# Optimization experiments

Measured on AMD Instinct MI355X. Metric: run time of the kernel, lower is better.

Reference implementation:

```python
import math
import jax, jax.numpy as jnp
import numpy as np

DIM = 1024
NUM_HEADS = 16
HEAD_DIM = DIM // NUM_HEADS
SCALE = HEAD_DIM ** -0.5
ROPE_BASE = 10000.0


def _rope(x):
    # x: [b, h, t, d]; rotate-half RoPE as in the torch module
    b, h, t, d = x.shape
    half = d // 2
    freqs = jnp.exp(-math.log(ROPE_BASE) * jnp.arange(half, dtype=jnp.float32) / half)
    pos = jnp.arange(t, dtype=jnp.float32)
    angles = pos[:, None] * freqs[None, :]          # [t, half]
    sin = jnp.sin(angles)[None, None, :, :]
    cos = jnp.cos(angles)[None, None, :, :]
    x1, x2 = x[..., :half], x[..., half:]
    return jnp.concatenate([x1 * cos - x2 * sin, x1 * sin + x2 * cos], axis=-1)


def setup_inputs() -> dict:
    key = jax.random.key(0)
    k1, k2, k3, k4 = jax.random.split(key, 4)
    b, t = 2, 2048
    x = jax.random.normal(k1, (b, t, DIM), dtype=jnp.float32)
    # nn.Linear(dim, 3*dim, bias=False): store as [in, out] for x @ W
    w_qkv = jax.random.normal(k2, (DIM, 3 * DIM), dtype=jnp.float32) * (DIM ** -0.5)
    w_proj = jax.random.normal(k3, (DIM, DIM), dtype=jnp.float32) * (DIM ** -0.5)
    b_proj = jax.random.normal(k4, (DIM,), dtype=jnp.float32) * 0.02
    return {"x": x, "w_qkv": w_qkv, "w_proj": w_proj, "b_proj": b_proj}


def reference(x, w_qkv, w_proj, b_proj):
    b, t, c = x.shape
    h, hd = NUM_HEADS, HEAD_DIM
    qkv = (x @ w_qkv).reshape(b, t, 3, h, hd)
    qkv = jnp.transpose(qkv, (2, 0, 3, 1, 4))      # [3, b, h, t, hd]
    q, k, v = qkv[0], qkv[1], qkv[2]
    q, k = _rope(q), _rope(k)
    attn = jnp.einsum('bhqd,bhkd->bhqk', q, k) * SCALE
    causal_mask = jnp.triu(jnp.ones((t, t), dtype=bool), k=1)
    attn = jnp.where(causal_mask[None, None], -jnp.inf, attn)
    attn = jax.nn.softmax(attn, axis=-1)
    out = jnp.einsum('bhqk,bhkd->bhqd', attn, v)
    out = jnp.transpose(out, (0, 2, 1, 3)).reshape(b, t, c)
    return out @ w_proj + b_proj
```

## Files before the change

kernel.cpp:

```cpp
#include <hip/hip_runtime.h>
#include <math.h>

typedef unsigned short u16;
typedef unsigned int u32;
typedef __bf16 bfrag8 __attribute__((ext_vector_type(8)));
typedef float f32x4 __attribute__((ext_vector_type(4)));

#define B_ 2
#define T_ 2048
#define H_ 16
#define D_ 64
#define C_ 1024
#define NQKV_ 3072

#define MFMA_BF16(a, b, c) __builtin_amdgcn_mfma_f32_16x16x32_bf16((a), (b), (c), 0, 0, 0)

__device__ __forceinline__ u16 f2bf(float f) {
  u32 u = __builtin_bit_cast(u32, f);
  u += 0x7fffu + ((u >> 16) & 1u);
  return (u16)(u >> 16);
}

__device__ __forceinline__ float exp2_fast(float x) {
#if __has_builtin(__builtin_amdgcn_exp2f)
  return __builtin_amdgcn_exp2f(x);
#else
  return __expf(x * 0.6931471805599453f);
#endif
}

__device__ __forceinline__ void load_lds16(const u16* gp, u16* lp) {
  __builtin_amdgcn_global_load_lds(
      (const __attribute__((address_space(1))) u32*)(const void*)gp,
      (__attribute__((address_space(3))) u32*)(void*)lp, 16, 0, 0);
}

__global__ __launch_bounds__(256) void prep(const float* __restrict__ x,
                                            u16* __restrict__ xb,
                                            const float* __restrict__ wqkv,
                                            u16* __restrict__ wqkvT,
                                            const float* __restrict__ wproj,
                                            u16* __restrict__ wprojT) {
  int bid = blockIdx.x;
  int tid = threadIdx.x;
  __shared__ u16 tile[64][65];
  if (bid < 2048) {
    size_t i = ((size_t)bid * 256 + tid) * 8;
    const float* s = x + i;
    float4 a = *(const float4*)s, b = *(const float4*)(s + 4);
    union { uint4 v; u16 h[8]; } t;
    t.h[0] = f2bf(a.x); t.h[1] = f2bf(a.y); t.h[2] = f2bf(a.z); t.h[3] = f2bf(a.w);
    t.h[4] = f2bf(b.x); t.h[5] = f2bf(b.y); t.h[6] = f2bf(b.z); t.h[7] = f2bf(b.w);
    *(uint4*)(xb + i) = t.v;
    return;
  }
  const float* src;
  u16* dst;
  int N, bx, by;
  if (bid < 2816) {
    int rel = bid - 2048;
    src = wqkv; dst = wqkvT; N = NQKV_;
    bx = (rel % 48) * 64; by = (rel / 48) * 64;
  } else {
    int rel = bid - 2816;
    src = wproj; dst = wprojT; N = C_;
    bx = (rel & 15) * 64; by = (rel >> 4) * 64;
  }
  for (int idx = tid; idx < 4096; idx += 256) {
    int r = idx >> 6, c = idx & 63;
    tile[r][c] = f2bf(src[(size_t)(by + r) * N + bx + c]);
  }
  __syncthreads();
  for (int idx = tid; idx < 4096; idx += 256) {
    int r = idx >> 6, c = idx & 63;
    dst[(size_t)(bx + r) * C_ + by + c] = tile[c][r];
  }
}

__global__ __launch_bounds__(256) void gemm_qkv_rope(const u16* __restrict__ X,
                                                     const u16* __restrict__ WT,
                                                     u16* __restrict__ qb,
                                                     u16* __restrict__ kb,
                                                     u16* __restrict__ vtb) {
  const int K = C_;
  __shared__ __align__(16) u16 As[2][128 * 64];
  __shared__ __align__(16) u16 Bs[2][128 * 64];
  int tid = threadIdx.x;
  int lane = tid & 63, wave = tid >> 6;
  int quad = lane >> 4, lr = lane & 15;
  int m0 = blockIdx.y * 128, n0 = blockIdx.x * 128;
  int wrow = (wave >> 1) * 64, wcol = (wave & 1) * 64;
  int r0 = wave * 32;
  int srow = lane >> 3;
  int schunk = (lane & 7) ^ srow;

  int koff0 = ((quad ^ (lr & 7)) << 3);
  int koff1 = (((4 | quad) ^ (lr & 7)) << 3);

  f32x4 zero = {0.f, 0.f, 0.f, 0.f};
  f32x4 acc[4][4];
#pragma unroll
  for (int i = 0; i < 4; i++)
#pragma unroll
    for (int j = 0; j < 4; j++) acc[i][j] = zero;

  const u16* ga = X + (size_t)(m0 + r0 + srow) * K + schunk * 8;
  const u16* gb = WT + (size_t)(n0 + r0 + srow) * K + schunk * 8;

#pragma unroll
  for (int l = 0; l < 4; l++) {
    load_lds16(ga + (size_t)(l * 8) * K, &As[0][(r0 + l * 8) * 64]);
    load_lds16(gb + (size_t)(l * 8) * K, &Bs[0][(r0 + l * 8) * 64]);
  }

  int buf = 0;
  for (int k0 = 0; k0 < K; k0 += 64) {
    __syncthreads();
    if (k0 + 64 < K) {
#pragma unroll
      for (int l = 0; l < 4; l++) {
        load_lds16(ga + (size_t)(l * 8) * K + k0 + 64, &As[buf ^ 1][(r0 + l * 8) * 64]);
        load_lds16(gb + (size_t)(l * 8) * K + k0 + 64, &Bs[buf ^ 1][(r0 + l * 8) * 64]);
      }
    }
    bfrag8 af[4][2], bf[4][2];
#pragma unroll
    for (int i = 0; i < 4; i++) {
      const u16* ar = &As[buf][(wrow + i * 16 + lr) * 64];
      af[i][0] = *(const bfrag8*)(ar + koff0);
      af[i][1] = *(const bfrag8*)(ar + koff1);
    }
#pragma unroll
    for (int j = 0; j < 4; j++) {
      const u16* br = &Bs[buf][(wcol + j * 16 + lr) * 64];
      bf[j][0] = *(const bfrag8*)(br + koff0);
      bf[j][1] = *(const bfrag8*)(br + koff1);
    }
#pragma unroll
    for (int i = 0; i < 4; i++)
#pragma unroll
      for (int j = 0; j < 4; j++) {
        acc[i][j] = MFMA_BF16(af[i][0], bf[j][0], acc[i][j]);
        acc[i][j] = MFMA_BF16(af[i][1], bf[j][1], acc[i][j]);
      }
    buf ^= 1;
  }

  int colbase = n0 + wcol;
  int which = colbase >> 10;
  int h = (colbase & 1023) >> 6;
  if (which < 2) {
    u16* dst = which == 0 ? qb : kb;
    float sc0 = (which == 0) ? 0.18033688011112042f : 1.0f;
    float fr0 = __expf(-0.28782313662425574f * (float)lr);
    float fr1 = __expf(-0.28782313662425574f * (float)(16 + lr));
#pragma unroll
    for (int i = 0; i < 4; i++) {
#pragma unroll
      for (int r = 0; r < 4; r++) {
        int m = m0 + wrow + i * 16 + quad * 4 + r;
        int b = m >> 11, tt = m & 2047;
        size_t base = ((size_t)(b * H_ + h) * T_ + tt) * D_;
        float sn, cs;
        __sincosf((float)tt * fr0, &sn, &cs);
        dst[base + lr] = f2bf((acc[i][0][r] * cs - acc[i][2][r] * sn) * sc0);
        dst[base + lr + 32] = f2bf((acc[i][0][r] * sn + acc[i][2][r] * cs) * sc0);
        __sincosf((float)tt * fr1, &sn, &cs);
        dst[base + 16 + lr] = f2bf((acc[i][1][r] * cs - acc[i][3][r] * sn) * sc0);
        dst[base + 48 + lr] = f2bf((acc[i][1][r] * sn + acc[i][3][r] * cs) * sc0);
      }
    }
  } else {
#pragma unroll
    for (int i = 0; i < 4; i++) {
      int mb = m0 + wrow + i * 16 + quad * 4;
      int b = mb >> 11, tt = mb & 2047;
      u16* vb = vtb + ((size_t)(b * H_ + h) * D_) * T_ + tt;
#pragma unroll
      for (int j = 0; j < 4; j++) {
        union { uint2 v; u16 hh[4]; } pk;
#pragma unroll
        for (int r = 0; r < 4; r++) pk.hh[r] = f2bf(acc[i][j][r]);
        *(uint2*)(vb + (size_t)(j * 16 + lr) * T_) = pk.v;
      }
    }
  }
}

__global__ __launch_bounds__(512) void attn_k(const u16* __restrict__ qb,
                                              const u16* __restrict__ kb,
                                              const u16* __restrict__ vtb,
                                              u16* __restrict__ ob) {
  __shared__ __align__(16) u16 Ks[2][64 * 64];
  __shared__ __align__(16) u16 Vt[2][64 * 64];
  __shared__ __align__(16) u16 Pst[8][16 * 72];
  int tid = threadIdx.x;
  int lane = tid & 63, wave = tid >> 6;
  int quad = lane >> 4, lr = lane & 15;
  int i = blockIdx.x;
  int bq = 15 - (i >> 5);
  int bh = i & 31;
  int b = bh >> 4, h = bh & 15;
  const u16* Q = qb + (size_t)bh * T_ * D_;
  const u16* Kp = kb + (size_t)bh * T_ * D_;
  const u16* Vp = vtb + (size_t)bh * D_ * T_;
  int qr0 = bq * 128 + wave * 16;
  int r0v = wave * 8;
  int sr = lane >> 3;
  int sc = (((lane & 7) ^ sr) * 8);

  int koff0 = ((quad ^ (lr & 7)) << 3);
  int koff1 = (((4 | quad) ^ (lr & 7)) << 3);

  bfrag8 qf[2];
#pragma unroll
  for (int ks = 0; ks < 2; ks++)
    qf[ks] = *(const bfrag8*)(Q + (size_t)(qr0 + lr) * D_ + ks * 32 + quad * 8);

  f32x4 zero = {0.f, 0.f, 0.f, 0.f};
  f32x4 o[4];
#pragma unroll
  for (int nn = 0; nn < 4; nn++) o[nn] = zero;
  float ps0 = 0.f, ps1 = 0.f, ps2 = 0.f, ps3 = 0.f;

  const u16* gk = Kp + (size_t)(r0v + sr) * D_ + sc;
  const u16* gv = Vp + (size_t)(r0v + sr) * T_ + sc;
  int niter = 2 * bq + 2;
  int wlast = 2 * bq + (wave >> 2);
  int qloc = (wave & 3) * 16 + lr;

  load_lds16(gk, &Ks[0][r0v * 64]);
  load_lds16(gv, &Vt[0][r0v * 64]);

  int buf = 0;
  for (int it = 0; it < niter; it++) {
    __syncthreads();
    if (it + 1 < niter) {
      int tkn = (it + 1) * 64;
      load_lds16(gk + (size_t)tkn * D_, &Ks[buf ^ 1][r0v * 64]);
      load_lds16(gv + tkn, &Vt[buf ^ 1][r0v * 64]);
    }
    if (it <= wlast) {
      const u16* ks_ = Ks[buf];
      const u16* vt_ = Vt[buf];

      f32x4 s[4];
#pragma unroll
      for (int j = 0; j < 4; j++) s[j] = zero;
#pragma unroll
      for (int j = 0; j < 4; j++) {
        bfrag8 kf0 = *(const bfrag8*)&ks_[(j * 16 + lr) * 64 + koff0];
        bfrag8 kf1 = *(const bfrag8*)&ks_[(j * 16 + lr) * 64 + koff1];
        s[j] = MFMA_BF16(kf0, qf[0], s[j]);
        s[j] = MFMA_BF16(kf1, qf[1], s[j]);
      }

      bool edge = (it == wlast);
#pragma unroll
      for (int j = 0; j < 4; j++) {
        float p[4];
#pragma unroll
        for (int r = 0; r < 4; r++) {
          float e = exp2_fast(s[j][r]);
          if (edge) {
            int kvloc = j * 16 + quad * 4 + r;
            e = (kvloc <= qloc) ? e : 0.f;
          }
          p[r] = e;
        }
        ps0 += p[0];
        ps1 += p[1];
        ps2 += p[2];
        ps3 += p[3];
        u32 u0 = __builtin_bit_cast(u32, p[0]) + 0x8000u;
        u32 u1 = __builtin_bit_cast(u32, p[1]) + 0x8000u;
        u32 u2 = __builtin_bit_cast(u32, p[2]) + 0x8000u;
        u32 u3 = __builtin_bit_cast(u32, p[3]) + 0x8000u;
        uint2 pk;
        pk.x = (u0 >> 16) | (u1 & 0xffff0000u);
        pk.y = (u2 >> 16) | (u3 & 0xffff0000u);
        *(uint2*)&Pst[wave][lr * 72 + j * 16 + quad * 4] = pk;
      }

#pragma unroll
      for (int ks = 0; ks < 2; ks++) {
        bfrag8 pf = *(const bfrag8*)&Pst[wave][lr * 72 + ks * 32 + quad * 8];
        int ko = ks ? koff1 : koff0;
#pragma unroll
        for (int nn = 0; nn < 4; nn++) {
          bfrag8 vf = *(const bfrag8*)&vt_[(nn * 16 + lr) * 64 + ko];
          o[nn] = MFMA_BF16(pf, vf, o[nn]);
        }
      }
    }
    buf ^= 1;
  }

  float l = (ps0 + ps1) + (ps2 + ps3);
  l += __shfl_xor(l, 16, 64);
  l += __shfl_xor(l, 32, 64);
  float linv = 1.0f / l;

#pragma unroll
  for (int r = 0; r < 4; r++) {
    float lrec = __shfl(linv, quad * 4 + r, 64);
    int row = qr0 + quad * 4 + r;
#pragma unroll
    for (int nn = 0; nn < 4; nn++)
      ob[(size_t)(b * T_ + row) * C_ + h * 64 + nn * 16 + lr] = f2bf(o[nn][r] * lrec);
  }
}

__global__ __launch_bounds__(256) void gemm_proj(const u16* __restrict__ A,
                                                 const u16* __restrict__ WT,
                                                 const float* __restrict__ bias,
                                                 float* __restrict__ out) {
  const int K = C_;
  __shared__ __align__(16) u16 As[2][64 * 64];
  __shared__ __align__(16) u16 Bs[2][128 * 64];
  int tid = threadIdx.x;
  int lane = tid & 63, wave = tid >> 6;
  int quad = lane >> 4, lr = lane & 15;
  int m0 = blockIdx.y * 64, n0 = blockIdx.x * 128;
  int wcol = wave * 32;
  int srow = lane >> 3;
  int schunk = (lane & 7) ^ srow;

  int koff0 = ((quad ^ (lr & 7)) << 3);
  int koff1 = (((4 | quad) ^ (lr & 7)) << 3);

  f32x4 zero = {0.f, 0.f, 0.f, 0.f};
  f32x4 acc[4][2];
#pragma unroll
  for (int i = 0; i < 4; i++)
#pragma unroll
    for (int j = 0; j < 2; j++) acc[i][j] = zero;

  const u16* ga = A + (size_t)(m0 + wave * 16 + srow) * K + schunk * 8;
  const u16* gb = WT + (size_t)(n0 + wave * 32 + srow) * K + schunk * 8;

  load_lds16(ga, &As[0][(wave * 16) * 64]);
  load_lds16(ga + (size_t)8 * K, &As[0][(wave * 16 + 8) * 64]);
#pragma unroll
  for (int l = 0; l < 4; l++)
    load_lds16(gb + (size_t)(l * 8) * K, &Bs[0][(wave * 32 + l * 8) * 64]);

  int buf = 0;
  for (int k0 = 0; k0 < K; k0 += 64) {
    __syncthreads();
    if (k0 + 64 < K) {
      load_lds16(ga + k0 + 64, &As[buf ^ 1][(wave * 16) * 64]);
      load_lds16(ga + (size_t)8 * K + k0 + 64, &As[buf ^ 1][(wave * 16 + 8) * 64]);
#pragma unroll
      for (int l = 0; l < 4; l++)
        load_lds16(gb + (size_t)(l * 8) * K + k0 + 64, &Bs[buf ^ 1][(wave * 32 + l * 8) * 64]);
    }
    bfrag8 af[4][2], bf[2][2];
#pragma unroll
    for (int i = 0; i < 4; i++) {
      const u16* ar = &As[buf][(i * 16 + lr) * 64];
      af[i][0] = *(const bfrag8*)(ar + koff0);
      af[i][1] = *(const bfrag8*)(ar + koff1);
    }
#pragma unroll
    for (int j = 0; j < 2; j++) {
      const u16* br = &Bs[buf][(wcol + j * 16 + lr) * 64];
      bf[j][0] = *(const bfrag8*)(br + koff0);
      bf[j][1] = *(const bfrag8*)(br + koff1);
    }
#pragma unroll
    for (int i = 0; i < 4; i++)
#pragma unroll
      for (int j = 0; j < 2; j++) {
        acc[i][j] = MFMA_BF16(af[i][0], bf[j][0], acc[i][j]);
        acc[i][j] = MFMA_BF16(af[i][1], bf[j][1], acc[i][j]);
      }
    buf ^= 1;
  }

#pragma unroll
  for (int i = 0; i < 4; i++)
#pragma unroll
    for (int r = 0; r < 4; r++) {
      int m = m0 + i * 16 + quad * 4 + r;
#pragma unroll
      for (int j = 0; j < 2; j++) {
        int n = n0 + wcol + j * 16 + lr;
        out[(size_t)m * C_ + n] = acc[i][j][r] + bias[n];
      }
    }
}

extern "C" void kernel_launch(void* const* d_in, const int* in_sizes, int n_in,
                              void* d_out, int out_size, void* d_ws, size_t ws_size,
                              hipStream_t stream) {
  const float* x = (const float*)d_in[0];
  const float* w_qkv = (const float*)d_in[1];
  const float* w_proj = (const float*)d_in[2];
  const float* b_proj = (const float*)d_in[3];

  char* w = (char*)d_ws;
  u16* xb = (u16*)(w + 256);
  u16* regA = xb + (size_t)4096 * 1024;
  u16* wqkvT = regA;
  u16* abuf = regA;
  u16* wprojT = regA + (size_t)4096 * 1024;
  u16* qbuf = wprojT + (size_t)1024 * 1024;
  u16* kbuf = qbuf + (size_t)B_ * H_ * T_ * D_;
  u16* vtb = kbuf + (size_t)B_ * H_ * T_ * D_;

  prep<<<3072, 256, 0, stream>>>(x, xb, w_qkv, wqkvT, w_proj, wprojT);
  gemm_qkv_rope<<<dim3(NQKV_ / 128, (B_ * T_) / 128), 256, 0, stream>>>(xb, wqkvT, qbuf, kbuf, vtb);
  attn_k<<<512, 512, 0, stream>>>(qbuf, kbuf, vtb, abuf);
  gemm_proj<<<dim3(C_ / 128, (B_ * T_) / 64), 256, 0, stream>>>(abuf, wprojT, b_proj, (float*)d_out);
}
```

Before: 187.2 us.

## Double KV tile size per barrier in attention and swizzle P staging buffer

After: 180.0 us (median of 2 runs). -3.9%, faster.

```diff
diff --git a/kernel.cpp b/kernel.cpp
--- a/kernel.cpp
+++ b/kernel.cpp
@@ -191,26 +191,33 @@
                                               const u16* __restrict__ kb,
                                               const u16* __restrict__ vtb,
                                               u16* __restrict__ ob) {
-  __shared__ __align__(16) u16 Ks[2][64 * 64];
-  __shared__ __align__(16) u16 Vt[2][64 * 64];
-  __shared__ __align__(16) u16 Pst[8][16 * 72];
+  __shared__ __align__(16) u16 Ks[2][128 * 64];
+  __shared__ __align__(16) u16 Vt[2][64 * 128];
+  __shared__ __align__(16) u16 Pst[8][16 * 64];
   int tid = threadIdx.x;
   int lane = tid & 63, wave = tid >> 6;
   int quad = lane >> 4, lr = lane & 15;
   int i = blockIdx.x;
   int bq = 15 - (i >> 5);
   int bh = i & 31;
-  int b = bh >> 4, h = bh & 15;
+  int b = bh >> 4, h2 = bh & 15;
   const u16* Q = qb + (size_t)bh * T_ * D_;
   const u16* Kp = kb + (size_t)bh * T_ * D_;
   const u16* Vp = vtb + (size_t)bh * D_ * T_;
   int qr0 = bq * 128 + wave * 16;
-  int r0v = wave * 8;
-  int sr = lane >> 3;
-  int sc = (((lane & 7) ^ sr) * 8);
+
+  int rK = lane >> 3;
+  int cK = ((lane & 7) ^ rK) * 8;
+  const u16* gk0 = Kp + (size_t)(wave * 16 + rK) * D_ + cK;
+  const u16* gk1 = gk0 + (size_t)8 * D_;
+  int rV = lane >> 4;
+  int cV = (lane & 15) ^ rV;
+  const u16* gv0 = Vp + (size_t)(wave * 8 + rV) * T_ + cV * 8;
+  const u16* gv1 = Vp + (size_t)(wave * 8 + 4 + rV) * T_ + (cV ^ 4) * 8;
 
   int koff0 = ((quad ^ (lr & 7)) << 3);
   int koff1 = (((4 | quad) ^ (lr & 7)) << 3);
+  int lsw = lr & 7;
 
   bfrag8 qf[2];
 #pragma unroll
@@ -223,73 +230,80 @@
   for (int nn = 0; nn < 4; nn++) o[nn] = zero;
   float ps0 = 0.f, ps1 = 0.f, ps2 = 0.f, ps3 = 0.f;
 
-  const u16* gk = Kp + (size_t)(r0v + sr) * D_ + sc;
-  const u16* gv = Vp + (size_t)(r0v + sr) * T_ + sc;
-  int niter = 2 * bq + 2;
+  int nkt = bq + 1;
   int wlast = 2 * bq + (wave >> 2);
   int qloc = (wave & 3) * 16 + lr;
 
-  load_lds16(gk, &Ks[0][r0v * 64]);
-  load_lds16(gv, &Vt[0][r0v * 64]);
+  load_lds16(gk0, &Ks[0][(wave * 16) * 64]);
+  load_lds16(gk1, &Ks[0][(wave * 16 + 8) * 64]);
+  load_lds16(gv0, &Vt[0][(wave * 8) * 128]);
+  load_lds16(gv1, &Vt[0][(wave * 8 + 4) * 128]);
 
   int buf = 0;
-  for (int it = 0; it < niter; it++) {
+  for (int kt = 0; kt < nkt; kt++) {
     __syncthreads();
-    if (it + 1 < niter) {
-      int tkn = (it + 1) * 64;
-      load_lds16(gk + (size_t)tkn * D_, &Ks[buf ^ 1][r0v * 64]);
-      load_lds16(gv + tkn, &Vt[buf ^ 1][r0v * 64]);
-    }
-    if (it <= wlast) {
-      const u16* ks_ = Ks[buf];
-      const u16* vt_ = Vt[buf];
-
-      f32x4 s[4];
-#pragma unroll
-      for (int j = 0; j < 4; j++) s[j] = zero;
-#pragma unroll
-      for (int j = 0; j < 4; j++) {
-        bfrag8 kf0 = *(const bfrag8*)&ks_[(j * 16 + lr) * 64 + koff0];
-        bfrag8 kf1 = *(const bfrag8*)&ks_[(j * 16 + lr) * 64 + koff1];
-        s[j] = MFMA_BF16(kf0, qf[0], s[j]);
-        s[j] = MFMA_BF16(kf1, qf[1], s[j]);
-      }
-
-      bool edge = (it == wlast);
-#pragma unroll
-      for (int j = 0; j < 4; j++) {
-        float p[4];
-#pragma unroll
-        for (int r = 0; r < 4; r++) {
-          float e = exp2_fast(s[j][r]);
-          if (edge) {
-            int kvloc = j * 16 + quad * 4 + r;
-            e = (kvloc <= qloc) ? e : 0.f;
+    if (kt + 1 < nkt) {
+      int tb = (kt + 1) * 128;
+      load_lds16(gk0 + (size_t)tb * D_, &Ks[buf ^ 1][(wave * 16) * 64]);
+      load_lds16(gk1 + (size_t)tb * D_, &Ks[buf ^ 1][(wave * 16 + 8) * 64]);
+      load_lds16(gv0 + tb, &Vt[buf ^ 1][(wave * 8) * 128]);
+      load_lds16(gv1 + tb, &Vt[buf ^ 1][(wave * 8 + 4) * 128]);
+    }
+    const u16* ks_ = Ks[buf];
+    const u16* vt_ = Vt[buf];
+#pragma unroll
+    for (int h = 0; h < 2; h++) {
+      int st = 2 * kt + h;
+      if (st <= wlast) {
+        f32x4 s[4];
+#pragma unroll
+        for (int j = 0; j < 4; j++) s[j] = zero;
+#pragma unroll
+        for (int j = 0; j < 4; j++) {
+          const u16* kr = &ks_[(h * 64 + j * 16 + lr) * 64];
+          bfrag8 kf0 = *(const bfrag8*)(kr + koff0);
+          bfrag8 kf1 = *(const bfrag8*)(kr + koff1);
+          s[j] = MFMA_BF16(kf0, qf[0], s[j]);
+          s[j] = MFMA_BF16(kf1, qf[1], s[j]);
+        }
+
+        bool edge = (st == wlast);
+#pragma unroll
+        for (int j = 0; j < 4; j++) {
+          float p[4];
+#pragma unroll
+          for (int r = 0; r < 4; r++) {
+            float e = exp2_fast(s[j][r]);
+            if (edge) {
+              int kvloc = j * 16 + quad * 4 + r;
+              e = (kvloc <= qloc) ? e : 0.f;
+            }
+            p[r] = e;
           }
-          p[r] = e;
+          ps0 += p[0];
+          ps1 += p[1];
+          ps2 += p[2];
+          ps3 += p[3];
+          u32 u0 = __builtin_bit_cast(u32, p[0]) + 0x8000u;
+          u32 u1 = __builtin_bit_cast(u32, p[1]) + 0x8000u;
+          u32 u2 = __builtin_bit_cast(u32, p[2]) + 0x8000u;
+          u32 u3 = __builtin_bit_cast(u32, p[3]) + 0x8000u;
+          uint2 pk;
+          pk.x = (u0 >> 16) | (u1 & 0xffff0000u);
+          pk.y = (u2 >> 16) | (u3 & 0xffff0000u);
+          *(uint2*)&Pst[wave][lr * 64 + (((2 * j + (quad >> 1)) ^ lsw) << 3) +
+                              ((quad & 1) << 2)] = pk;
         }
-        ps0 += p[0];
-        ps1 += p[1];
-        ps2 += p[2];
-        ps3 += p[3];
-        u32 u0 = __builtin_bit_cast(u32, p[0]) + 0x8000u;
-        u32 u1 = __builtin_bit_cast(u32, p[1]) + 0x8000u;
-        u32 u2 = __builtin_bit_cast(u32, p[2]) + 0x8000u;
-        u32 u3 = __builtin_bit_cast(u32, p[3]) + 0x8000u;
-        uint2 pk;
-        pk.x = (u0 >> 16) | (u1 & 0xffff0000u);
-        pk.y = (u2 >> 16) | (u3 & 0xffff0000u);
-        *(uint2*)&Pst[wave][lr * 72 + j * 16 + quad * 4] = pk;
-      }
-
-#pragma unroll
-      for (int ks = 0; ks < 2; ks++) {
-        bfrag8 pf = *(const bfrag8*)&Pst[wave][lr * 72 + ks * 32 + quad * 8];
-        int ko = ks ? koff1 : koff0;
-#pragma unroll
-        for (int nn = 0; nn < 4; nn++) {
-          bfrag8 vf = *(const bfrag8*)&vt_[(nn * 16 + lr) * 64 + ko];
-          o[nn] = MFMA_BF16(pf, vf, o[nn]);
+
+#pragma unroll
+        for (int ks = 0; ks < 2; ks++) {
+          bfrag8 pf = *(const bfrag8*)&Pst[wave][lr * 64 + (((4 * ks + quad) ^ lsw) << 3)];
+#pragma unroll
+          for (int nn = 0; nn < 4; nn++) {
+            int vko = ((8 * h + 4 * ks + quad) ^ lsw) << 3;
+            bfrag8 vf = *(const bfrag8*)&vt_[(nn * 16 + lr) * 128 + vko];
+            o[nn] = MFMA_BF16(pf, vf, o[nn]);
+          }
         }
       }
     }
@@ -307,7 +321,7 @@
     int row = qr0 + quad * 4 + r;
 #pragma unroll
     for (int nn = 0; nn < 4; nn++)
-      ob[(size_t)(b * T_ + row) * C_ + h * 64 + nn * 16 + lr] = f2bf(o[nn][r] * lrec);
+      ob[(size_t)(b * T_ + row) * C_ + h2 * 64 + nn * 16 + lr] = f2bf(o[nn][r] * lrec);
   }
 }
 
```
